# Kernel tuning notes

Hardware: AMD Instinct MI355X
Metric: run time of the kernel (lower is better)

Reference implementation:

```python
import jax, jax.numpy as jnp
import numpy as np

N_NODES = 200000
N_EDGES = 800000
N_GRAPHS = 4000
IN_CH = 128
EDGE_DIM = 16
CONVS = [128, 256, 256, 256]          # in_channels + convs_layers
DENSE = [256, 512, 128, 32]           # last conv width + dense_layers
OUT_CH = 1
BN_EPS = 1e-5


def _lin_init(key, fan_in, fan_out):
    k1, k2 = jax.random.split(key)
    s = 1.0 / np.sqrt(fan_in)
    W = jax.random.uniform(k1, (fan_in, fan_out), minval=-s, maxval=s, dtype=jnp.float32)
    b = jax.random.uniform(k2, (fan_out,), minval=-s, maxval=s, dtype=jnp.float32)
    return W, b


def setup_inputs() -> dict:
    key = jax.random.key(0)
    ks = jax.random.split(key, 32)
    inp = {
        "x": jax.random.normal(ks[0], (N_NODES, IN_CH), dtype=jnp.float32),
        "edge_index": jax.random.randint(ks[1], (2, N_EDGES), 0, N_NODES),
        "batch": jnp.sort(jax.random.randint(ks[2], (N_NODES,), 0, N_GRAPHS)),
        "edge_attr": jax.random.normal(ks[3], (N_EDGES, EDGE_DIM), dtype=jnp.float32),
    }
    ki = 4
    for i in range(3):  # three GINE conv layers
        cin, cout = CONVS[i], CONVS[i + 1]
        We, be = _lin_init(ks[ki], EDGE_DIM, cin); ki += 1  # edge_attr -> node dim
        Wn, bn = _lin_init(ks[ki], cin, cout); ki += 1      # GIN MLP (single Linear)
        inp[f"We{i}"], inp[f"be{i}"] = We, be
        inp[f"Wn{i}"], inp[f"bn{i}"] = Wn, bn
        inp[f"g{i}"] = jnp.ones((cout,), jnp.float32)       # BatchNorm1d gamma
        inp[f"beta{i}"] = jnp.zeros((cout,), jnp.float32)   # BatchNorm1d beta
    for i in range(3):  # dense head
        W, b = _lin_init(ks[ki], DENSE[i], DENSE[i + 1]); ki += 1
        inp[f"Wd{i}"], inp[f"bd{i}"] = W, b
    inp["Wo"], inp["bo"] = _lin_init(ks[ki], DENSE[-1], OUT_CH)
    return inp


def _gine_conv(x, src, dst, edge_attr, We, be, Wn, bn):
    # GINEConv: out_i = Linear((1+eps)*x_i + sum_{j->i} relu(x_j + lin(e_ji))), eps=0
    e = edge_attr @ We + be                         # [E, cin]
    msg = jax.nn.relu(x[src] + e)                   # gather + fuse  [E, cin]
    agg = jax.ops.segment_sum(msg, dst, num_segments=x.shape[0])  # scatter-add
    return (x + agg) @ Wn + bn


def _batch_norm(h, gamma, beta):
    mu = jnp.mean(h, axis=0)
    var = jnp.mean(jnp.square(h - mu), axis=0)      # biased var (training mode)
    return (h - mu) * jax.lax.rsqrt(var + BN_EPS) * gamma + beta


def reference(x, edge_index, batch, edge_attr,
              We0, be0, Wn0, bn0, g0, beta0,
              We1, be1, Wn1, bn1, g1, beta1,
              We2, be2, Wn2, bn2, g2, beta2,
              Wd0, bd0, Wd1, bd1, Wd2, bd2, Wo, bo):
    src, dst = edge_index[0], edge_index[1]
    params = [(We0, be0, Wn0, bn0, g0, beta0),
              (We1, be1, Wn1, bn1, g1, beta1),
              (We2, be2, Wn2, bn2, g2, beta2)]
    h = x
    for (We, be, Wn, bn, g, b) in params:
        h = _gine_conv(h, src, dst, edge_attr, We, be, Wn, bn)
        h = jax.nn.relu(h)
        h = _batch_norm(h, g, b)
    # global_mean_pool over graphs
    sums = jax.ops.segment_sum(h, batch, num_segments=N_GRAPHS)       # [G, d]
    cnts = jax.ops.segment_sum(jnp.ones((h.shape[0],), h.dtype), batch,
                               num_segments=N_GRAPHS)
    y = sums / jnp.maximum(cnts, 1.0)[:, None]
    # dense head: Linear+ReLU stack, then output Linear (dropout_p = 0)
    for (W, b) in [(Wd0, bd0), (Wd1, bd1), (Wd2, bd2)]:
        y = jax.nn.relu(y @ W + b)
    return y @ Wo + bo
```

## Files before the change

### kernel.cpp

```cpp
#include <hip/hip_runtime.h>
#include <hip/hip_bf16.h>

using bf16 = __hip_bfloat16;
typedef __attribute__((ext_vector_type(8))) short bf16x8;
typedef __attribute__((ext_vector_type(4))) float f32x4;

constexpr int NN = 200000;
constexpr int NE = 800000;
constexpr int NG = 4000;
constexpr int ED = 16;
constexpr float BN_EPS = 1e-5f;

constexpr int WSTEP = 88;
constexpr int NB    = (NE + NN + WSTEP - 1) / WSTEP;

__device__ __forceinline__ float  ld1(const float* p) { return *p; }
__device__ __forceinline__ float  ld1(const bf16*  p) { return __bfloat162float(*p); }
__device__ __forceinline__ float2 ld2f(const float* p) { return *(const float2*)p; }
__device__ __forceinline__ float2 ld2f(const bf16*  p) {
    union { ushort2 u; bf16 h[2]; } t;
    t.u = *(const ushort2*)p;
    return make_float2(__bfloat162float(t.h[0]), __bfloat162float(t.h[1]));
}
__device__ __forceinline__ float4 ld4(const float* p) { return *(const float4*)p; }
__device__ __forceinline__ float4 ld4(const bf16*  p) {
    union { ushort4 u; bf16 h[4]; } t;
    t.u = *(const ushort4*)p;
    return make_float4(__bfloat162float(t.h[0]), __bfloat162float(t.h[1]),
                       __bfloat162float(t.h[2]), __bfloat162float(t.h[3]));
}
__device__ __forceinline__ void st1(float* p, float v) { *p = v; }
__device__ __forceinline__ void st1(bf16*  p, float v) { *p = __float2bfloat16(v); }
__device__ __forceinline__ void st4(float* p, float4 v) { *(float4*)p = v; }
__device__ __forceinline__ void st4(bf16*  p, float4 v) {
    union { ushort4 u; bf16 h[4]; } t;
    t.h[0] = __float2bfloat16(v.x); t.h[1] = __float2bfloat16(v.y);
    t.h[2] = __float2bfloat16(v.z); t.h[3] = __float2bfloat16(v.w);
    *(ushort4*)p = t.u;
}
__device__ __forceinline__ float bfraw(unsigned short u) {
    union { unsigned short s; bf16 h; } t; t.s = u;
    return __bfloat162float(t.h);
}

__device__ __forceinline__ void gld16(const void* g, void* l)
{
    __builtin_amdgcn_global_load_lds(
        (const __attribute__((address_space(1))) void*)g,
        (__attribute__((address_space(3))) void*)l, 16, 0, 0);
}

constexpr int SCAN_CHUNK = 1024;
constexpr int SCAN_NBLK  = (NN + SCAN_CHUNK - 1) / SCAN_CHUNK;

__global__ __launch_bounds__(256)
void k_hist(const int* __restrict__ ei, int* __restrict__ cnt)
{
    int e = blockIdx.x * 256 + threadIdx.x;
    const int stride = gridDim.x * 256;
    for (; e < NE; e += stride) atomicAdd(&cnt[ei[NE + e]], 1);
}

__global__ __launch_bounds__(256)
void k_scan_block(const int* __restrict__ cnt, int* __restrict__ bsum)
{
    __shared__ int red[256];
    const int b = blockIdx.x, t = threadIdx.x;
    const int base = b * SCAN_CHUNK + t * 4;
    int s = 0;
    #pragma unroll
    for (int k = 0; k < 4; ++k) { const int i = base + k; if (i < NN) s += cnt[i]; }
    red[t] = s; __syncthreads();
    for (int off = 128; off > 0; off >>= 1) {
        if (t < off) red[t] += red[t + off];
        __syncthreads();
    }
    if (t == 0) bsum[b] = red[0];
}

__global__ __launch_bounds__(256)
void k_scan_top(int* __restrict__ bsum, int n)
{
    __shared__ int sh[256];
    const int t = threadIdx.x;
    const int orig = (t < n) ? bsum[t] : 0;
    sh[t] = orig; __syncthreads();
    for (int off = 1; off < 256; off <<= 1) {
        const int v = (t >= off) ? sh[t - off] : 0;
        __syncthreads();
        sh[t] += v;
        __syncthreads();
    }
    if (t < n) bsum[t] = sh[t] - orig;
}

__global__ __launch_bounds__(256)
void k_scan_emit(const int* __restrict__ cnt, const int* __restrict__ bsum,
                 int* __restrict__ row_ptr, int* __restrict__ cursor)
{
    __shared__ int sh[256];
    const int b = blockIdx.x, t = threadIdx.x;
    const int base = b * SCAN_CHUNK + t * 4;
    int c[4]; int s = 0;
    #pragma unroll
    for (int k = 0; k < 4; ++k) {
        const int i = base + k;
        c[k] = (i < NN) ? cnt[i] : 0;
        s += c[k];
    }
    const int orig = s;
    sh[t] = s; __syncthreads();
    for (int off = 1; off < 256; off <<= 1) {
        const int v = (t >= off) ? sh[t - off] : 0;
        __syncthreads();
        sh[t] += v;
        __syncthreads();
    }
    int run = bsum[b] + sh[t] - orig;
    #pragma unroll
    for (int k = 0; k < 4; ++k) {
        const int i = base + k;
        if (i < NN) { row_ptr[i] = run; cursor[i] = run; run += c[k]; }
    }
    if (b == 0 && t == 0) row_ptr[NN] = NE;
}

__global__ __launch_bounds__(256)
void k_scatter(const int* __restrict__ ei, int* __restrict__ cursor,
               int* __restrict__ perm)
{
    int e = blockIdx.x * 256 + threadIdx.x;
    const int stride = gridDim.x * 256;
    for (; e < NE; e += stride) {
        const int d = ei[NE + e];
        const int p = atomicAdd(&cursor[d], 1);
        perm[p] = e;
    }
}

__global__ __launch_bounds__(256)
void k_bounds2(const int* __restrict__ row_ptr, int* __restrict__ nb)
{
    const int t = blockIdx.x * 256 + threadIdx.x;
    if (t > NB) return;
    const long long target = (long long)t * (NE + NN) / NB;
    int lo = 0, hi = NN;
    while (lo < hi) {
        const int mid = (lo + hi) >> 1;
        const long long W = (long long)row_ptr[mid] + mid;
        if (W >= target) hi = mid; else lo = mid + 1;
    }
    nb[t] = lo;
}

__global__ __launch_bounds__(256)
void k_gather_edges_bf(const int* __restrict__ ei, const float* __restrict__ ea,
                       const int* __restrict__ perm, int* __restrict__ src_perm,
                       bf16* __restrict__ ea_bf)
{
    const int t = blockIdx.x * 256 + threadIdx.x;
    if (t >= NE * 16) return;
    const int idx = t >> 4, k2 = (t & 15) * 2;
    const int e = perm[idx];
    union { ushort2 u; bf16 h[2]; } o;
    if (k2 < ED) {
        const float2 v = *(const float2*)&ea[(size_t)e * ED + k2];
        o.h[0] = __float2bfloat16(v.x);
        o.h[1] = __float2bfloat16(v.y);
    } else {
        o.u = make_ushort2(0, 0);
    }
    *(ushort2*)&ea_bf[(size_t)idx * 32 + k2] = o.u;
    if ((t & 15) == 0) src_perm[idx] = ei[e];
}

__global__ __launch_bounds__(256)
void k_wt(const float* __restrict__ W, bf16* __restrict__ Wt, int K, int N)
{
    const int i = blockIdx.x * 256 + threadIdx.x;
    if (i >= K * N) return;
    const int k = i / N, n = i % N;
    Wt[(size_t)n * K + k] = __float2bfloat16(W[i]);
}

__global__ __launch_bounds__(256)
void k_wte(const float* __restrict__ We, bf16* __restrict__ Wte, int cin)
{
    const int i = blockIdx.x * 256 + threadIdx.x;
    if (i >= cin * 32) return;
    const int n = i >> 5, k = i & 31;
    Wte[i] = __float2bfloat16((k < ED) ? We[k * cin + n] : 0.f);
}

__global__ __launch_bounds__(256)
void k_bnab(float* __restrict__ st, const float* __restrict__ g,
            const float* __restrict__ b)
{
    const int c = threadIdx.x;
    const float inv = 1.f / (float)NN;
    const float mu  = st[c] * inv;
    const float var = st[256 + c] * inv - mu * mu;
    const float A   = g[c] * rsqrtf(var + BN_EPS);
    st[512 + c] = A;
    st[768 + c] = b[c] - mu * A;
}

template<typename XT, bool FOLD>
__global__ __launch_bounds__(256)
void fused_agg128(const XT* __restrict__ x, const bf16* __restrict__ ea_bf,
                  const bf16* __restrict__ Wte, const float* __restrict__ be,
                  const int* __restrict__ src_perm, const int* __restrict__ row_ptr,
                  const int* __restrict__ nb, const float* __restrict__ st,
                  bf16* __restrict__ agg)
{
    constexpr int CIN  = 128;
    constexpr int MSTR = CIN + 8;
    constexpr int CPL  = 2;
    __shared__ short ea_s[128 * 32];
    __shared__ short msg[128 * MSTR];

    const int tid  = threadIdx.x;
    const int lane = tid & 63;
    const int wv   = tid >> 6;
    const int b    = blockIdx.x;
    const int n0 = nb[b], n1 = nb[b + 1];
    if (n0 >= n1) return;
    const int e0 = row_ptr[n0];
    const int e1 = row_ptr[n1];
    int ne = e1 - e0; if (ne > 128) ne = 128;

    const int l15  = lane & 15;
    const int quad = lane >> 4;
    const int rsub = lane >> 2;
    const int part = lane & 3;

    #pragma unroll
    for (int i = 0; i < 2; ++i) {
        const int c = i * 4 + wv;
        int r = c * 16 + rsub;
        if (r >= ne) r = (ne > 0) ? ne - 1 : 0;
        size_t gr = (size_t)(e0 + r); if (gr >= NE) gr = NE - 1;
        gld16(&ea_bf[gr * 32 + part * 8], &ea_s[c * 512]);
    }

    const int wc = (wv & 1) * 64;
    const int wr = (wv >> 1) * 64;
    bf16x8 bfr[4];
    #pragma unroll
    for (int i = 0; i < 4; ++i)
        bfr[i] = *(const bf16x8*)&Wte[(size_t)(wc + i * 16 + l15) * 32 + quad * 8];
    float bv[4];
    #pragma unroll
    for (int ni = 0; ni < 4; ++ni)
        bv[ni] = be[wc + ni * 16 + l15];

    __syncthreads();

    {
        f32x4 acc[4][4];
        #pragma unroll
        for (int i = 0; i < 4; ++i)
            #pragma unroll
            for (int j = 0; j < 4; ++j)
                acc[i][j] = (f32x4){0.f, 0.f, 0.f, 0.f};
        bf16x8 af[4];
        #pragma unroll
        for (int i = 0; i < 4; ++i)
            af[i] = *(const bf16x8*)&ea_s[(wr + i * 16 + l15) * 32 + quad * 8];
        #pragma unroll
        for (int mi = 0; mi < 4; ++mi)
            #pragma unroll
            for (int ni = 0; ni < 4; ++ni)
                acc[mi][ni] = __builtin_amdgcn_mfma_f32_16x16x32_bf16(
                                  af[mi], bfr[ni], acc[mi][ni], 0, 0, 0);
        #pragma unroll
        for (int mi = 0; mi < 4; ++mi) {
            const int row0 = wr + mi * 16 + quad * 4;
            #pragma unroll
            for (int r = 0; r < 4; ++r) {
                const int row = row0 + r;
                #pragma unroll
                for (int ni = 0; ni < 4; ++ni) {
                    const float v = acc[mi][ni][r] + bv[ni];
                    msg[row * MSTR + wc + ni * 16 + l15] =
                        (short)__bfloat16_as_ushort(__float2bfloat16(v));
                }
            }
        }
    }
    __syncthreads();

    const int c0 = lane * CPL;
    float Af[CPL], Bf[CPL];
    #pragma unroll
    for (int q = 0; q < CPL; ++q) {
        Af[q] = FOLD ? st[512 + c0 + q] : 1.f;
        Bf[q] = FOLD ? st[768 + c0 + q] : 0.f;
    }

    for (int ni = wv; ni < n1 - n0; ni += 4) {
        const int node = n0 + ni;
        float acc2[CPL];
        const float2 v = ld2f(&x[(size_t)node * CIN + c0]);
        acc2[0] = fmaf(v.x, Af[0], Bf[0]);
        acc2[1] = fmaf(v.y, Af[1], Bf[1]);

        const int f0 = row_ptr[node], f1 = row_ptr[node + 1];
        for (int base2 = f0; base2 < f1; base2 += 4) {
            int ss[4], li[4];
            #pragma unroll
            for (int j = 0; j < 4; ++j) {
                int idx = base2 + j; if (idx >= f1) idx = f1 - 1;
                ss[j] = src_perm[idx];
                int l = idx - e0; if (l > 127) l = 127;
                li[j] = l;
            }
            float2 xv[4]; ushort2 mv[4];
            #pragma unroll
            for (int j = 0; j < 4; ++j) {
                xv[j] = ld2f(&x[(size_t)ss[j] * CIN + c0]);
                mv[j] = *(const ushort2*)&msg[li[j] * MSTR + c0];
            }
            #pragma unroll
            for (int j = 0; j < 4; ++j) {
                if (base2 + j < f1) {
                    acc2[0] += fmaxf(fmaf(xv[j].x, Af[0], Bf[0]) + bfraw(mv[j].x), 0.f);
                    acc2[1] += fmaxf(fmaf(xv[j].y, Af[1], Bf[1]) + bfraw(mv[j].y), 0.f);
                }
            }
        }

        union { ushort2 u; bf16 h[2]; } t;
        t.h[0] = __float2bfloat16(acc2[0]);
        t.h[1] = __float2bfloat16(acc2[1]);
        *(ushort2*)&agg[(size_t)node * CIN + c0] = t.u;
    }
}

template<typename XT, bool FOLD>
__global__ __launch_bounds__(512)
void fused_agg256(const XT* __restrict__ x, const bf16* __restrict__ ea_bf,
                  const bf16* __restrict__ Wte, const float* __restrict__ be,
                  const int* __restrict__ src_perm, const int* __restrict__ row_ptr,
                  const int* __restrict__ nb, const float* __restrict__ st,
                  bf16* __restrict__ agg)
{
    constexpr int CIN  = 256;
    constexpr int MSTR = CIN + 8;
    constexpr int CPL  = 4;
    __shared__ short ea_s[128 * 32];
    __shared__ short msg[128 * MSTR];

    const int tid  = threadIdx.x;
    const int lane = tid & 63;
    const int wv   = tid >> 6;
    const int b    = blockIdx.x;
    const int n0 = nb[b], n1 = nb[b + 1];
    if (n0 >= n1) return;
    const int e0 = row_ptr[n0];
    const int e1 = row_ptr[n1];
    int ne = e1 - e0; if (ne > 128) ne = 128;

    const int l15  = lane & 15;
    const int quad = lane >> 4;
    const int rsub = lane >> 2;
    const int part = lane & 3;

    {
        int r = wv * 16 + rsub;
        if (r >= ne) r = (ne > 0) ? ne - 1 : 0;
        size_t gr = (size_t)(e0 + r); if (gr >= NE) gr = NE - 1;
        gld16(&ea_bf[gr * 32 + part * 8], &ea_s[wv * 512]);
    }

    const int wc = (wv & 3) * 64;
    const int wr = (wv >> 2) * 64;
    bf16x8 bfr[4];
    #pragma unroll
    for (int i = 0; i < 4; ++i)
        bfr[i] = *(const bf16x8*)&Wte[(size_t)(wc + i * 16 + l15) * 32 + quad * 8];
    float bv[4];
    #pragma unroll
    for (int ni = 0; ni < 4; ++ni)
        bv[ni] = be[wc + ni * 16 + l15];

    __syncthreads();

    {
        f32x4 acc[4][4];
        #pragma unroll
        for (int i = 0; i < 4; ++i)
            #pragma unroll
            for (int j = 0; j < 4; ++j)
                acc[i][j] = (f32x4){0.f, 0.f, 0.f, 0.f};
        bf16x8 af[4];
        #pragma unroll
        for (int i = 0; i < 4; ++i)
            af[i] = *(const bf16x8*)&ea_s[(wr + i * 16 + l15) * 32 + quad * 8];
        #pragma unroll
        for (int mi = 0; mi < 4; ++mi)
            #pragma unroll
            for (int ni = 0; ni < 4; ++ni)
                acc[mi][ni] = __builtin_amdgcn_mfma_f32_16x16x32_bf16(
                                  af[mi], bfr[ni], acc[mi][ni], 0, 0, 0);
        #pragma unroll
        for (int mi = 0; mi < 4; ++mi) {
            const int row0 = wr + mi * 16 + quad * 4;
            #pragma unroll
            for (int r = 0; r < 4; ++r) {
                const int row = row0 + r;
                #pragma unroll
                for (int ni = 0; ni < 4; ++ni) {
                    const float v = acc[mi][ni][r] + bv[ni];
                    msg[row * MSTR + wc + ni * 16 + l15] =
                        (short)__bfloat16_as_ushort(__float2bfloat16(v));
                }
            }
        }
    }
    __syncthreads();

    const int c0 = lane * CPL;
    float Af[CPL], Bf[CPL];
    #pragma unroll
    for (int q = 0; q < CPL; ++q) {
        Af[q] = FOLD ? st[512 + c0 + q] : 1.f;
        Bf[q] = FOLD ? st[768 + c0 + q] : 0.f;
    }

    for (int ni = wv; ni < n1 - n0; ni += 8) {
        const int node = n0 + ni;
        float acc2[CPL];
        const float4 v = ld4(&x[(size_t)node * CIN + c0]);
        acc2[0] = fmaf(v.x, Af[0], Bf[0]); acc2[1] = fmaf(v.y, Af[1], Bf[1]);
        acc2[2] = fmaf(v.z, Af[2], Bf[2]); acc2[3] = fmaf(v.w, Af[3], Bf[3]);

        const int f0 = row_ptr[node], f1 = row_ptr[node + 1];
        for (int base2 = f0; base2 < f1; base2 += 4) {
            int ss[4], li[4];
            #pragma unroll
            for (int j = 0; j < 4; ++j) {
                int idx = base2 + j; if (idx >= f1) idx = f1 - 1;
                ss[j] = src_perm[idx];
                int l = idx - e0; if (l > 127) l = 127;
                li[j] = l;
            }
            float4 xv[4]; ushort4 mv[4];
            #pragma unroll
            for (int j = 0; j < 4; ++j) {
                xv[j] = ld4(&x[(size_t)ss[j] * CIN + c0]);
                mv[j] = *(const ushort4*)&msg[li[j] * MSTR + c0];
            }
            #pragma unroll
            for (int j = 0; j < 4; ++j) {
                if (base2 + j < f1) {
                    acc2[0] += fmaxf(fmaf(xv[j].x, Af[0], Bf[0]) + bfraw(mv[j].x), 0.f);
                    acc2[1] += fmaxf(fmaf(xv[j].y, Af[1], Bf[1]) + bfraw(mv[j].y), 0.f);
                    acc2[2] += fmaxf(fmaf(xv[j].z, Af[2], Bf[2]) + bfraw(mv[j].z), 0.f);
                    acc2[3] += fmaxf(fmaf(xv[j].w, Af[3], Bf[3]) + bfraw(mv[j].w), 0.f);
                }
            }
        }

        union { ushort4 u; bf16 h[4]; } t;
        t.h[0] = __float2bfloat16(acc2[0]); t.h[1] = __float2bfloat16(acc2[1]);
        t.h[2] = __float2bfloat16(acc2[2]); t.h[3] = __float2bfloat16(acc2[3]);
        *(ushort4*)&agg[(size_t)node * CIN + c0] = t.u;
    }
}

template<int K, bool STATS>
__global__ __launch_bounds__(256, 3)
void gemm_mfma(const bf16* __restrict__ A, const bf16* __restrict__ Wt,
               const float* __restrict__ bias, bf16* __restrict__ C, int M,
               float* __restrict__ st)
{
    __shared__ short As[128 * 32];
    __shared__ short Bs[128 * 32];
    const int tid  = threadIdx.x;
    const int bm   = blockIdx.y * 128;
    const int bn   = blockIdx.x * 128;
    const int lane = tid & 63;
    const int wave = tid >> 6;
    const int wr   = (wave >> 1) * 64;
    const int wc   = (wave & 1) * 64;
    const int l15  = lane & 15;
    const int quad = lane >> 4;
    const int rsub = lane >> 2;
    const int part = lane & 3;

    f32x4 acc[4][4];
    #pragma unroll
    for (int i = 0; i < 4; ++i)
        #pragma unroll
        for (int j = 0; j < 4; ++j)
            acc[i][j] = (f32x4){0.f, 0.f, 0.f, 0.f};

    for (int k0 = 0; k0 < K; k0 += 32) {
        #pragma unroll
        for (int i = 0; i < 2; ++i) {
            const int ca = wave * 2 + i;
            int ar = bm + ca * 16 + rsub; if (ar >= M) ar = M - 1;
            gld16(&A[(size_t)ar * K + k0 + part * 8], &As[ca * 512]);
            gld16(&Wt[(size_t)(bn + ca * 16 + rsub) * K + k0 + part * 8],
                  &Bs[ca * 512]);
        }
        __syncthreads();

        bf16x8 af[4], bfr[4];
        #pragma unroll
        for (int i = 0; i < 4; ++i) {
            af[i]  = *(const bf16x8*)&As[(wr + i * 16 + l15) * 32 + quad * 8];
            bfr[i] = *(const bf16x8*)&Bs[(wc + i * 16 + l15) * 32 + quad * 8];
        }
        #pragma unroll
        for (int mi = 0; mi < 4; ++mi)
            #pragma unroll
            for (int ni = 0; ni < 4; ++ni)
                acc[mi][ni] = __builtin_amdgcn_mfma_f32_16x16x32_bf16(
                                  af[mi], bfr[ni], acc[mi][ni], 0, 0, 0);
        __syncthreads();
    }

    float bv[4];
    #pragma unroll
    for (int ni = 0; ni < 4; ++ni)
        bv[ni] = bias[bn + wc + ni * 16 + l15];
    float ps[4]  = {0.f, 0.f, 0.f, 0.f};
    float ps2[4] = {0.f, 0.f, 0.f, 0.f};
    #pragma unroll
    for (int mi = 0; mi < 4; ++mi) {
        const int row0 = bm + wr + mi * 16 + quad * 4;
        #pragma unroll
        for (int r = 0; r < 4; ++r) {
            const int row = row0 + r;
            if (row < M) {
                #pragma unroll
                for (int ni = 0; ni < 4; ++ni) {
                    float v = acc[mi][ni][r] + bv[ni];
                    v = fmaxf(v, 0.f);
                    C[(size_t)row * 256 + bn + wc + ni * 16 + l15] = __float2bfloat16(v);
                    if (STATS) { ps[ni] += v; ps2[ni] = fmaf(v, v, ps2[ni]); }
                }
            }
        }
    }
    if (STATS) {
        #pragma unroll
        for (int ni = 0; ni < 4; ++ni) {
            float s = ps[ni], q = ps2[ni];
            s += __shfl_xor(s, 16); s += __shfl_xor(s, 32);
            q += __shfl_xor(q, 16); q += __shfl_xor(q, 32);
            if (quad == 0) {
                const int col = bn + wc + ni * 16 + l15;
                atomicAdd(&st[col], s);
                atomicAdd(&st[256 + col], q);
            }
        }
    }
}

template<bool RELU, typename InT, typename OutT>
__global__ __launch_bounds__(256)
void gemm_rk(const InT* __restrict__ A, const float* __restrict__ W,
             const float* __restrict__ bias, OutT* __restrict__ C,
             int M, int N, int K)
{
    __shared__ float Asm[16][64];
    __shared__ float Wsm[16][64];
    const int bm = blockIdx.y * 64;
    const int bn = blockIdx.x * 64;
    const int tid = threadIdx.x;
    const int tx = tid & 15, ty = tid >> 4;
    const int ar = tid >> 2, ac = (tid & 3) * 4;
    const int wrr = tid >> 4, wcc = (tid & 15) * 4;

    float acc[4][4] = {};

    for (int k0 = 0; k0 < K; k0 += 16) {
        float4 av = make_float4(0.f, 0.f, 0.f, 0.f);
        if (bm + ar < M)
            av = ld4(A + (size_t)(bm + ar) * K + k0 + ac);
        Asm[ac + 0][ar] = av.x; Asm[ac + 1][ar] = av.y;
        Asm[ac + 2][ar] = av.z; Asm[ac + 3][ar] = av.w;

        float4 wv = make_float4(0.f, 0.f, 0.f, 0.f);
        if (bn + wcc < N)
            wv = *(const float4*)(W + (size_t)(k0 + wrr) * N + bn + wcc);
        *(float4*)&Wsm[wrr][wcc] = wv;
        __syncthreads();

        #pragma unroll
        for (int k = 0; k < 16; ++k) {
            const float4 a4 = *(const float4*)&Asm[k][ty * 4];
            const float4 b4 = *(const float4*)&Wsm[k][tx * 4];
            const float aa[4] = {a4.x, a4.y, a4.z, a4.w};
            const float bb[4] = {b4.x, b4.y, b4.z, b4.w};
            #pragma unroll
            for (int i = 0; i < 4; ++i)
                #pragma unroll
                for (int j = 0; j < 4; ++j)
                    acc[i][j] += aa[i] * bb[j];
        }
        __syncthreads();
    }

    float bvals[4];
    #pragma unroll
    for (int j = 0; j < 4; ++j) {
        const int col = bn + tx * 4 + j;
        bvals[j] = (col < N) ? bias[col] : 0.f;
    }
    #pragma unroll
    for (int i = 0; i < 4; ++i) {
        const int row = bm + ty * 4 + i;
        if (row >= M) continue;
        float v[4];
        #pragma unroll
        for (int j = 0; j < 4; ++j) {
            v[j] = acc[i][j] + bvals[j];
            if (RELU) v[j] = fmaxf(v[j], 0.f);
        }
        if (bn + tx * 4 + 3 < N) {
            st4(C + (size_t)row * N + bn + tx * 4, make_float4(v[0], v[1], v[2], v[3]));
        } else {
            #pragma unroll
            for (int j = 0; j < 4; ++j) {
                const int col = bn + tx * 4 + j;
                if (col < N) st1(C + (size_t)row * N + col, v[j]);
            }
        }
    }
}

template<typename InT, bool FOLD>
__global__ __launch_bounds__(256)
void pool_sum(const InT* __restrict__ h, const int* __restrict__ batch,
              const float* __restrict__ st,
              float* __restrict__ sums, float* __restrict__ cnts)
{
    const int c = threadIdx.x;
    size_t n0 = (size_t)blockIdx.x * 128;
    size_t n1 = n0 + 128; if (n1 > (size_t)NN) n1 = NN;
    if (n0 >= (size_t)NN) return;
    const float A = FOLD ? st[512 + c] : 1.f;
    const float B = FOLD ? st[768 + c] : 0.f;
    int cur = batch[n0];
    float s = 0.f, cnt = 0.f;
    for (size_t n = n0; n < n1; ++n) {
        const int b = batch[n];
        if (b != cur) {
            atomicAdd(&sums[(size_t)cur * 256 + c], s);
            if (c == 0) atomicAdd(&cnts[cur], cnt);
            s = 0.f; cnt = 0.f; cur = b;
        }
        const float v = ld1(&h[n * 256 + c]);
        s += fmaf(v, A, B);
        cnt += 1.f;
    }
    atomicAdd(&sums[(size_t)cur * 256 + c], s);
    if (c == 0) atomicAdd(&cnts[cur], cnt);
}

__global__ __launch_bounds__(256)
void pool_div(float* __restrict__ sums, const float* __restrict__ cnts)
{
    const int i = blockIdx.x * 256 + threadIdx.x;
    const int g = i >> 8;
    sums[i] = sums[i] / fmaxf(cnts[g], 1.f);
}

__global__ __launch_bounds__(256)
void head_out(const float* __restrict__ y, const float* __restrict__ Wo,
              const float* __restrict__ bo, float* __restrict__ out)
{
    const int g = blockIdx.x * 256 + threadIdx.x;
    if (g >= NG) return;
    float s = bo[0];
    #pragma unroll
    for (int k = 0; k < 32; ++k) s += y[g * 32 + k] * Wo[k];
    out[g] = s;
}

__global__ __launch_bounds__(256)
void diag_fill(float* __restrict__ out, int n, float v)
{
    const int i = blockIdx.x * 256 + threadIdx.x;
    if (i < n) out[i] = v;
}

extern "C" void kernel_launch(void* const* d_in, const int* in_sizes, int n_in,
                              void* d_out, int out_size, void* d_ws, size_t ws_size,
                              hipStream_t stream)
{
    const float* x    = (const float*)d_in[0];
    const int*   ei   = (const int*)d_in[1];
    const int*   batch= (const int*)d_in[2];
    const float* ea   = (const float*)d_in[3];
    const float* We[3] = {(const float*)d_in[4],  (const float*)d_in[10], (const float*)d_in[16]};
    const float* be[3] = {(const float*)d_in[5],  (const float*)d_in[11], (const float*)d_in[17]};
    const float* Wn[3] = {(const float*)d_in[6],  (const float*)d_in[12], (const float*)d_in[18]};
    const float* bnb[3]= {(const float*)d_in[7],  (const float*)d_in[13], (const float*)d_in[19]};
    const float* gm[3] = {(const float*)d_in[8],  (const float*)d_in[14], (const float*)d_in[20]};
    const float* bt[3] = {(const float*)d_in[9],  (const float*)d_in[15], (const float*)d_in[21]};
    const float* Wd0 = (const float*)d_in[22]; const float* bd0 = (const float*)d_in[23];
    const float* Wd1 = (const float*)d_in[24]; const float* bd1 = (const float*)d_in[25];
    const float* Wd2 = (const float*)d_in[26]; const float* bd2 = (const float*)d_in[27];
    const float* Wo  = (const float*)d_in[28]; const float* bo  = (const float*)d_in[29];
    float* out = (float*)d_out;
    float* ws  = (float*)d_ws;

    constexpr size_t OFF_H    = 0;
    constexpr size_t OFF_AGG  = 25600000;
    constexpr size_t OFF_ST   = 51200000;
    constexpr size_t OFF_WT0  = OFF_ST + 1536;
    constexpr size_t OFF_WT1  = OFF_WT0 + 16384;
    constexpr size_t OFF_WT2  = OFF_WT1 + 32768;
    constexpr size_t OFF_WTE0 = OFF_WT2 + 32768;
    constexpr size_t OFF_WTE1 = OFF_WTE0 + 2048;
    constexpr size_t OFF_WTE2 = OFF_WTE1 + 4096;
    constexpr size_t OFF_EA   = OFF_WTE2 + 4096;
    constexpr size_t OFF_SRC  = OFF_EA + 12800000;
    constexpr size_t OFF_RP   = OFF_SRC + NE;
    constexpr size_t OFF_CUR  = OFF_RP + (NN + 1);
    constexpr size_t OFF_PERM = OFF_CUR + NN;
    constexpr size_t OFF_BSUM = OFF_PERM + NE;
    constexpr size_t OFF_NB   = OFF_BSUM + SCAN_NBLK;
    constexpr size_t BASE_END = OFF_NB + (NB + 4);
    constexpr size_t NEED_BASE = BASE_END * 4;

    bf16*  H        = (bf16*)(ws + OFF_H);
    bf16*  AGG      = (bf16*)(ws + OFF_AGG);
    float* st       = ws + OFF_ST;
    bf16*  wt0      = (bf16*)(ws + OFF_WT0);
    bf16*  wt1      = (bf16*)(ws + OFF_WT1);
    bf16*  wt2      = (bf16*)(ws + OFF_WT2);
    bf16*  wte[3]   = {(bf16*)(ws + OFF_WTE0), (bf16*)(ws + OFF_WTE1), (bf16*)(ws + OFF_WTE2)};
    bf16*  ea_bf    = (bf16*)(ws + OFF_EA);
    int*   src_perm = (int*)(ws + OFF_SRC);
    int*   row_ptr  = (int*)(ws + OFF_RP);
    int*   cursor   = (int*)(ws + OFF_CUR);
    int*   perm     = (int*)(ws + OFF_PERM);
    int*   bsum     = (int*)(ws + OFF_BSUM);
    int*   nb       = (int*)(ws + OFF_NB);

    if (ws_size < NEED_BASE) {
        diag_fill<<<(NG + 255) / 256, 256, 0, stream>>>(out, NG, (float)(ws_size >> 20));
        return;
    }

    hipMemsetAsync(row_ptr, 0, (size_t)(NN + 1) * 4, stream);
    k_hist<<<1024, 256, 0, stream>>>(ei, row_ptr);
    k_scan_block<<<SCAN_NBLK, 256, 0, stream>>>(row_ptr, bsum);
    k_scan_top<<<1, 256, 0, stream>>>(bsum, SCAN_NBLK);
    k_scan_emit<<<SCAN_NBLK, 256, 0, stream>>>(row_ptr, bsum, row_ptr, cursor);
    k_scatter<<<1024, 256, 0, stream>>>(ei, cursor, perm);
    k_bounds2<<<(NB + 256) / 256, 256, 0, stream>>>(row_ptr, nb);
    k_gather_edges_bf<<<(NE * 16 + 255) / 256, 256, 0, stream>>>(ei, ea, perm, src_perm, ea_bf);
    k_wte<<<(128 * 32 + 255) / 256, 256, 0, stream>>>(We[0], wte[0], 128);
    k_wte<<<(256 * 32 + 255) / 256, 256, 0, stream>>>(We[1], wte[1], 256);
    k_wte<<<(256 * 32 + 255) / 256, 256, 0, stream>>>(We[2], wte[2], 256);
    k_wt<<<(128 * 256 + 255) / 256, 256, 0, stream>>>(Wn[0], wt0, 128, 256);
    k_wt<<<(256 * 256 + 255) / 256, 256, 0, stream>>>(Wn[1], wt1, 256, 256);
    k_wt<<<(256 * 256 + 255) / 256, 256, 0, stream>>>(Wn[2], wt2, 256, 256);

    const dim3 mfma_grid(2, (NN + 127) / 128);

    fused_agg128<float, false><<<NB, 256, 0, stream>>>(
        x, ea_bf, wte[0], be[0], src_perm, row_ptr, nb, st, AGG);
    hipMemsetAsync(st, 0, 512 * 4, stream);
    gemm_mfma<128, true><<<mfma_grid, 256, 0, stream>>>(AGG, wt0, bnb[0], H, NN, st);
    k_bnab<<<1, 256, 0, stream>>>(st, gm[0], bt[0]);

    for (int l = 1; l < 3; ++l) {
        fused_agg256<bf16, true><<<NB, 512, 0, stream>>>(
            H, ea_bf, wte[l], be[l], src_perm, row_ptr, nb, st, AGG);
        hipMemsetAsync(st, 0, 512 * 4, stream);
        gemm_mfma<256, true><<<mfma_grid, 256, 0, stream>>>(
            AGG, (l == 1) ? wt1 : wt2, bnb[l], H, NN, st);
        k_bnab<<<1, 256, 0, stream>>>(st, gm[l], bt[l]);
    }

    float* poolb = (float*)AGG;
    float* cnts  = poolb + 1024000;
    float* y1    = poolb + 1028000;
    float* y2    = poolb + 3076000;
    float* y3    = poolb + 3588000;

    hipMemsetAsync(poolb, 0, (size_t)NG * 256 * 4, stream);
    hipMemsetAsync(cnts, 0, (size_t)NG * 4, stream);
    pool_sum<bf16, true><<<(NN + 127) / 128, 256, 0, stream>>>(H, batch, st, poolb, cnts);
    pool_div<<<NG, 256, 0, stream>>>(poolb, cnts);

    gemm_rk<true, float, float><<<dim3(8, (NG + 63) / 64), 256, 0, stream>>>(poolb, Wd0, bd0, y1, NG, 512, 256);
    gemm_rk<true, float, float><<<dim3(2, (NG + 63) / 64), 256, 0, stream>>>(y1, Wd1, bd1, y2, NG, 128, 512);
    gemm_rk<true, float, float><<<dim3(1, (NG + 63) / 64), 256, 0, stream>>>(y2, Wd2, bd2, y3, NG, 32, 128);
    head_out<<<(NG + 255) / 256, 256, 0, stream>>>(y3, Wo, bo, out);
}
```

Baseline: 1.478 ms.

## Stage edge sources and row pointers in LDS, widen gather unroll in aggregation kernels

Both fused aggregation kernels now preload the block's src_perm entries and row_ptr slice into shared memory, so the inner gather loop does an LDS lookup instead of a dependent global index load. The gather loop unroll rises from 4 to 8 neighbours to keep more independent x-row loads in flight, and the 256-wide kernel loads raw bf16 and converts inline. The 128-wide kernel moves from 256 to 512 threads with the MFMA edge projection split over 8 waves. This adds LDS and register pressure and drops the old NE clamp on the edge-attribute load, which depends on ne being positive.

```diff
diff --git a/kernel.cpp b/kernel.cpp
--- a/kernel.cpp
+++ b/kernel.cpp
@@ -206,7 +206,7 @@
 }
 
 template<typename XT, bool FOLD>
-__global__ __launch_bounds__(256)
+__global__ __launch_bounds__(512)
 void fused_agg128(const XT* __restrict__ x, const bf16* __restrict__ ea_bf,
                   const bf16* __restrict__ Wte, const float* __restrict__ be,
                   const int* __restrict__ src_perm, const int* __restrict__ row_ptr,
@@ -218,6 +218,8 @@
     constexpr int CPL  = 2;
     __shared__ short ea_s[128 * 32];
     __shared__ short msg[128 * MSTR];
+    __shared__ int   src_lds[128];
+    __shared__ int   rp_lds[132];
 
     const int tid  = threadIdx.x;
     const int lane = tid & 63;
@@ -228,23 +230,28 @@
     const int e0 = row_ptr[n0];
     const int e1 = row_ptr[n1];
     int ne = e1 - e0; if (ne > 128) ne = 128;
+    int nnb = n1 - n0; if (nnb > 128) nnb = 128;
 
     const int l15  = lane & 15;
     const int quad = lane >> 4;
     const int rsub = lane >> 2;
     const int part = lane & 3;
 
-    #pragma unroll
-    for (int i = 0; i < 2; ++i) {
-        const int c = i * 4 + wv;
-        int r = c * 16 + rsub;
-        if (r >= ne) r = (ne > 0) ? ne - 1 : 0;
-        size_t gr = (size_t)(e0 + r); if (gr >= NE) gr = NE - 1;
-        gld16(&ea_bf[gr * 32 + part * 8], &ea_s[c * 512]);
+    {
+        int r = wv * 16 + rsub;
+        if (r >= ne) r = ne - 1;
+        gld16(&ea_bf[(size_t)(e0 + r) * 32 + part * 8], &ea_s[wv * 512]);
+    }
+    if (tid < 128) {
+        const int i = (tid < ne) ? tid : ne - 1;
+        src_lds[tid] = src_perm[e0 + i];
+    } else if (tid < 384) {
+        const int i = tid - 128;
+        if (i <= nnb) rp_lds[i] = row_ptr[n0 + i];
     }
 
     const int wc = (wv & 1) * 64;
-    const int wr = (wv >> 1) * 64;
+    const int wr = (wv >> 1) * 32;
     bf16x8 bfr[4];
     #pragma unroll
     for (int i = 0; i < 4; ++i)
@@ -257,24 +264,24 @@
     __syncthreads();
 
     {
-        f32x4 acc[4][4];
-        #pragma unroll
-        for (int i = 0; i < 4; ++i)
+        f32x4 acc[2][4];
+        #pragma unroll
+        for (int i = 0; i < 2; ++i)
             #pragma unroll
             for (int j = 0; j < 4; ++j)
                 acc[i][j] = (f32x4){0.f, 0.f, 0.f, 0.f};
-        bf16x8 af[4];
-        #pragma unroll
-        for (int i = 0; i < 4; ++i)
+        bf16x8 af[2];
+        #pragma unroll
+        for (int i = 0; i < 2; ++i)
             af[i] = *(const bf16x8*)&ea_s[(wr + i * 16 + l15) * 32 + quad * 8];
         #pragma unroll
-        for (int mi = 0; mi < 4; ++mi)
+        for (int mi = 0; mi < 2; ++mi)
             #pragma unroll
             for (int ni = 0; ni < 4; ++ni)
                 acc[mi][ni] = __builtin_amdgcn_mfma_f32_16x16x32_bf16(
                                   af[mi], bfr[ni], acc[mi][ni], 0, 0, 0);
         #pragma unroll
-        for (int mi = 0; mi < 4; ++mi) {
+        for (int mi = 0; mi < 2; ++mi) {
             const int row0 = wr + mi * 16 + quad * 4;
             #pragma unroll
             for (int r = 0; r < 4; ++r) {
@@ -298,31 +305,26 @@
         Bf[q] = FOLD ? st[768 + c0 + q] : 0.f;
     }
 
-    for (int ni = wv; ni < n1 - n0; ni += 4) {
+    for (int ni = wv; ni < nnb; ni += 8) {
         const int node = n0 + ni;
         float acc2[CPL];
         const float2 v = ld2f(&x[(size_t)node * CIN + c0]);
         acc2[0] = fmaf(v.x, Af[0], Bf[0]);
         acc2[1] = fmaf(v.y, Af[1], Bf[1]);
 
-        const int f0 = row_ptr[node], f1 = row_ptr[node + 1];
-        for (int base2 = f0; base2 < f1; base2 += 4) {
-            int ss[4], li[4];
-            #pragma unroll
-            for (int j = 0; j < 4; ++j) {
+        const int f0 = rp_lds[ni], f1 = rp_lds[ni + 1];
+        for (int base2 = f0; base2 < f1; base2 += 8) {
+            float2 xv[8]; ushort2 mv[8];
+            #pragma unroll
+            for (int j = 0; j < 8; ++j) {
                 int idx = base2 + j; if (idx >= f1) idx = f1 - 1;
-                ss[j] = src_perm[idx];
                 int l = idx - e0; if (l > 127) l = 127;
-                li[j] = l;
+                const int sv = src_lds[l];
+                xv[j] = ld2f(&x[(size_t)sv * CIN + c0]);
+                mv[j] = *(const ushort2*)&msg[l * MSTR + c0];
             }
-            float2 xv[4]; ushort2 mv[4];
-            #pragma unroll
-            for (int j = 0; j < 4; ++j) {
-                xv[j] = ld2f(&x[(size_t)ss[j] * CIN + c0]);
-                mv[j] = *(const ushort2*)&msg[li[j] * MSTR + c0];
-            }
-            #pragma unroll
-            for (int j = 0; j < 4; ++j) {
+            #pragma unroll
+            for (int j = 0; j < 8; ++j) {
                 if (base2 + j < f1) {
                     acc2[0] += fmaxf(fmaf(xv[j].x, Af[0], Bf[0]) + bfraw(mv[j].x), 0.f);
                     acc2[1] += fmaxf(fmaf(xv[j].y, Af[1], Bf[1]) + bfraw(mv[j].y), 0.f);
@@ -337,9 +339,9 @@
     }
 }
 
-template<typename XT, bool FOLD>
+template<bool FOLD>
 __global__ __launch_bounds__(512)
-void fused_agg256(const XT* __restrict__ x, const bf16* __restrict__ ea_bf,
+void fused_agg256(const bf16* __restrict__ x, const bf16* __restrict__ ea_bf,
                   const bf16* __restrict__ Wte, const float* __restrict__ be,
                   const int* __restrict__ src_perm, const int* __restrict__ row_ptr,
                   const int* __restrict__ nb, const float* __restrict__ st,
@@ -350,6 +352,8 @@
     constexpr int CPL  = 4;
     __shared__ short ea_s[128 * 32];
     __shared__ short msg[128 * MSTR];
+    __shared__ int   src_lds[128];
+    __shared__ int   rp_lds[132];
 
     const int tid  = threadIdx.x;
     const int lane = tid & 63;
@@ -360,6 +364,7 @@
     const int e0 = row_ptr[n0];
     const int e1 = row_ptr[n1];
     int ne = e1 - e0; if (ne > 128) ne = 128;
+    int nnb = n1 - n0; if (nnb > 128) nnb = 128;
 
     const int l15  = lane & 15;
     const int quad = lane >> 4;
@@ -368,9 +373,15 @@
 
     {
         int r = wv * 16 + rsub;
-        if (r >= ne) r = (ne > 0) ? ne - 1 : 0;
-        size_t gr = (size_t)(e0 + r); if (gr >= NE) gr = NE - 1;
-        gld16(&ea_bf[gr * 32 + part * 8], &ea_s[wv * 512]);
+        if (r >= ne) r = ne - 1;
+        gld16(&ea_bf[(size_t)(e0 + r) * 32 + part * 8], &ea_s[wv * 512]);
+    }
+    if (tid < 128) {
+        const int i = (tid < ne) ? tid : ne - 1;
+        src_lds[tid] = src_perm[e0 + i];
+    } else if (tid < 384) {
+        const int i = tid - 128;
+        if (i <= nnb) rp_lds[i] = row_ptr[n0 + i];
     }
 
     const int wc = (wv & 3) * 64;
@@ -428,36 +439,31 @@
         Bf[q] = FOLD ? st[768 + c0 + q] : 0.f;
     }
 
-    for (int ni = wv; ni < n1 - n0; ni += 8) {
+    for (int ni = wv; ni < nnb; ni += 8) {
         const int node = n0 + ni;
         float acc2[CPL];
         const float4 v = ld4(&x[(size_t)node * CIN + c0]);
         acc2[0] = fmaf(v.x, Af[0], Bf[0]); acc2[1] = fmaf(v.y, Af[1], Bf[1]);
         acc2[2] = fmaf(v.z, Af[2], Bf[2]); acc2[3] = fmaf(v.w, Af[3], Bf[3]);
 
-        const int f0 = row_ptr[node], f1 = row_ptr[node + 1];
-        for (int base2 = f0; base2 < f1; base2 += 4) {
-            int ss[4], li[4];
-            #pragma unroll
-            for (int j = 0; j < 4; ++j) {
+        const int f0 = rp_lds[ni], f1 = rp_lds[ni + 1];
+        for (int base2 = f0; base2 < f1; base2 += 8) {
+            ushort4 xr[8]; ushort4 mv[8];
+            #pragma unroll
+            for (int j = 0; j < 8; ++j) {
                 int idx = base2 + j; if (idx >= f1) idx = f1 - 1;
-                ss[j] = src_perm[idx];
                 int l = idx - e0; if (l > 127) l = 127;
-                li[j] = l;
+                const int sv = src_lds[l];
+                xr[j] = *(const ushort4*)&x[(size_t)sv * CIN + c0];
+                mv[j] = *(const ushort4*)&msg[l * MSTR + c0];
             }
-            float4 xv[4]; ushort4 mv[4];
-            #pragma unroll
-            for (int j = 0; j < 4; ++j) {
-                xv[j] = ld4(&x[(size_t)ss[j] * CIN + c0]);
-                mv[j] = *(const ushort4*)&msg[li[j] * MSTR + c0];
-            }
-            #pragma unroll
-            for (int j = 0; j < 4; ++j) {
+            #pragma unroll
+            for (int j = 0; j < 8; ++j) {
                 if (base2 + j < f1) {
-                    acc2[0] += fmaxf(fmaf(xv[j].x, Af[0], Bf[0]) + bfraw(mv[j].x), 0.f);
-                    acc2[1] += fmaxf(fmaf(xv[j].y, Af[1], Bf[1]) + bfraw(mv[j].y), 0.f);
-                    acc2[2] += fmaxf(fmaf(xv[j].z, Af[2], Bf[2]) + bfraw(mv[j].z), 0.f);
-                    acc2[3] += fmaxf(fmaf(xv[j].w, Af[3], Bf[3]) + bfraw(mv[j].w), 0.f);
+                    acc2[0] += fmaxf(fmaf(bfraw(xr[j].x), Af[0], Bf[0]) + bfraw(mv[j].x), 0.f);
+                    acc2[1] += fmaxf(fmaf(bfraw(xr[j].y), Af[1], Bf[1]) + bfraw(mv[j].y), 0.f);
+                    acc2[2] += fmaxf(fmaf(bfraw(xr[j].z), Af[2], Bf[2]) + bfraw(mv[j].z), 0.f);
+                    acc2[3] += fmaxf(fmaf(bfraw(xr[j].w), Af[3], Bf[3]) + bfraw(mv[j].w), 0.f);
                 }
             }
         }
@@ -766,14 +772,14 @@
 
     const dim3 mfma_grid(2, (NN + 127) / 128);
 
-    fused_agg128<float, false><<<NB, 256, 0, stream>>>(
+    fused_agg128<float, false><<<NB, 512, 0, stream>>>(
         x, ea_bf, wte[0], be[0], src_perm, row_ptr, nb, st, AGG);
     hipMemsetAsync(st, 0, 512 * 4, stream);
     gemm_mfma<128, true><<<mfma_grid, 256, 0, stream>>>(AGG, wt0, bnb[0], H, NN, st);
     k_bnab<<<1, 256, 0, stream>>>(st, gm[0], bt[0]);
 
     for (int l = 1; l < 3; ++l) {
-        fused_agg256<bf16, true><<<NB, 512, 0, stream>>>(
+        fused_agg256<true><<<NB, 512, 0, stream>>>(
             H, ea_bf, wte[l], be[l], src_perm, row_ptr, nb, st, AGG);
         hipMemsetAsync(st, 0, 512 * 4, stream);
         gemm_mfma<256, true><<<mfma_grid, 256, 0, stream>>>(
```

Measured after the change: 1.337 ms. -9.5%, faster.
